# Performance work log

Measured on AMD Instinct MI355X. Metric: run time of the kernel, lower is better.

## Reference

```python
import jax, jax.numpy as jnp
import numpy as np

N = 50000
E = 800000
IN_FT = 256
OUT_FT = 64


def setup_inputs() -> dict:
    key = jax.random.key(0)
    k_seq, k_w, k_src, k_dst, k_val = jax.random.split(key, 5)
    seq = jax.random.normal(k_seq, (N, IN_FT), dtype=jnp.float32)
    # xavier_uniform_ for fc.weight [out_ft, in_ft]
    limit = float(np.sqrt(6.0 / (IN_FT + OUT_FT)))
    W = jax.random.uniform(k_w, (OUT_FT, IN_FT), minval=-limit, maxval=limit, dtype=jnp.float32)
    bias = jnp.zeros((OUT_FT,), dtype=jnp.float32)          # bias.data.fill_(0.0)
    alpha = jnp.full((1,), 0.25, dtype=jnp.float32)         # PReLU default init
    edge_src = jax.random.randint(k_src, (E,), 0, N, dtype=jnp.int32)
    edge_dst = jax.random.randint(k_dst, (E,), 0, N, dtype=jnp.int32)
    edge_val = jax.random.uniform(k_val, (E,), dtype=jnp.float32)
    return {"seq": seq, "W": W, "bias": bias, "alpha": alpha,
            "edge_src": edge_src, "edge_dst": edge_dst, "edge_val": edge_val}


def reference(seq, W, bias, alpha, edge_src, edge_dst, edge_val):
    # fc(seq): [N, in_ft] @ [in_ft, out_ft] -> [N, out_ft]
    fts = jnp.einsum('ni,oi->no', seq, W)
    # spmm(adj, fts): gather source features, scale by edge value, scatter-add to dst
    msgs = fts[edge_src] * edge_val[:, None]                # [E, out_ft]
    out = jax.ops.segment_sum(msgs, edge_dst, num_segments=seq.shape[0])
    out = out + bias
    # PReLU with scalar (single-channel) alpha
    return jnp.where(out >= 0, out, alpha * out)
```

## Files before the change

### kernel.cpp

```cpp
#include <hip/hip_runtime.h>
#include <hip/hip_fp16.h>

#define IN_FT 256
#define OUT_FT 64

constexpr int BIN_LOG   = 7;
constexpr int BIN_NODES = 1 << BIN_LOG;
constexpr int MAX_NBIN  = 512;
constexpr int BIN_CAP   = 2560;

typedef _Float16 half8 __attribute__((ext_vector_type(8)));
typedef float    f32x4 __attribute__((ext_vector_type(4)));

__global__ __launch_bounds__(256) void gemm_mfma(
    const float* __restrict__ seq, const float* __restrict__ W,
    __half* __restrict__ fts, int N, int* __restrict__ binCursor, int NBIN)
{
    const int t = (int)threadIdx.x;
    if (blockIdx.x == 0) {
        for (int i = t; i < NBIN; i += 256) binCursor[i] = 0;
    }

    __shared__ half8 Wh[4 * 8 * 64];

#pragma unroll
    for (int i = 0; i < 8; ++i) {
        int item = i * 256 + t;
        int l  = item & 63;
        int kc = (item >> 6) & 7;
        int nt = item >> 9;
        int m  = l & 15;
        int q  = l >> 4;
        const float* wp = W + (size_t)(nt * 16 + m) * IN_FT + kc * 32 + q * 8;
        float4 w0 = *(const float4*)wp;
        float4 w1 = *(const float4*)(wp + 4);
        half8 h;
        h[0] = (_Float16)w0.x; h[1] = (_Float16)w0.y;
        h[2] = (_Float16)w0.z; h[3] = (_Float16)w0.w;
        h[4] = (_Float16)w1.x; h[5] = (_Float16)w1.y;
        h[6] = (_Float16)w1.z; h[7] = (_Float16)w1.w;
        Wh[item] = h;
    }
    __syncthreads();

    const int wave = t >> 6;
    const int l    = t & 63;
    int nodeBase = (int)blockIdx.x * 64 + wave * 16;
    const bool active = (nodeBase < N);
    if (nodeBase > N - 16) nodeBase = N - 16;
    const int m = l & 15;
    const int q = l >> 4;
    const float* ap = seq + (size_t)(nodeBase + m) * IN_FT + q * 8;

    f32x4 acc0 = {0.f, 0.f, 0.f, 0.f};
    f32x4 acc1 = {0.f, 0.f, 0.f, 0.f};
    f32x4 acc2 = {0.f, 0.f, 0.f, 0.f};
    f32x4 acc3 = {0.f, 0.f, 0.f, 0.f};

    float4 a0 = *(const float4*)(ap);
    float4 a1 = *(const float4*)(ap + 4);

#pragma unroll
    for (int kc = 0; kc < 8; ++kc) {
        float4 c0 = a0, c1 = a1;
        if (kc < 7) {
            a0 = *(const float4*)(ap + (kc + 1) * 32);
            a1 = *(const float4*)(ap + (kc + 1) * 32 + 4);
        }
        half8 af;
        af[0] = (_Float16)c0.x; af[1] = (_Float16)c0.y;
        af[2] = (_Float16)c0.z; af[3] = (_Float16)c0.w;
        af[4] = (_Float16)c1.x; af[5] = (_Float16)c1.y;
        af[6] = (_Float16)c1.z; af[7] = (_Float16)c1.w;

        half8 b0 = Wh[(0 * 8 + kc) * 64 + l];
        half8 b1 = Wh[(1 * 8 + kc) * 64 + l];
        half8 b2 = Wh[(2 * 8 + kc) * 64 + l];
        half8 b3 = Wh[(3 * 8 + kc) * 64 + l];
        acc0 = __builtin_amdgcn_mfma_f32_16x16x32_f16(af, b0, acc0, 0, 0, 0);
        acc1 = __builtin_amdgcn_mfma_f32_16x16x32_f16(af, b1, acc1, 0, 0, 0);
        acc2 = __builtin_amdgcn_mfma_f32_16x16x32_f16(af, b2, acc2, 0, 0, 0);
        acc3 = __builtin_amdgcn_mfma_f32_16x16x32_f16(af, b3, acc3, 0, 0, 0);
    }

    if (active) {
#pragma unroll
        for (int r = 0; r < 4; ++r) {
            int node = nodeBase + q * 4 + r;
            __half* op = fts + (size_t)node * OUT_FT + m;
            op[0]  = __float2half(acc0[r]);
            op[16] = __float2half(acc1[r]);
            op[32] = __float2half(acc2[r]);
            op[48] = __float2half(acc3[r]);
        }
    }
}

__global__ __launch_bounds__(256) void bin_scatter(
    const int* __restrict__ src, const int* __restrict__ dst,
    const float* __restrict__ val, int* __restrict__ binCursor,
    int2* __restrict__ binned, int E, int NBIN)
{
    __shared__ int h[MAX_NBIN];
    __shared__ int base[MAX_NBIN];
    const int t = (int)threadIdx.x;
    for (int i = t; i < NBIN; i += 256) h[i] = 0;
    __syncthreads();
    const int chunk = (E + (int)gridDim.x - 1) / (int)gridDim.x;
    const int s0 = (int)blockIdx.x * chunk;
    const int e0 = min(s0 + chunk, E);
    for (int i = s0 + t; i < e0; i += 256) atomicAdd(&h[dst[i] >> BIN_LOG], 1);
    __syncthreads();
    for (int i = t; i < NBIN; i += 256) {
        int c = h[i];
        base[i] = c ? atomicAdd(&binCursor[i], c) : 0;
        h[i] = 0;
    }
    __syncthreads();
    for (int i = s0 + t; i < e0; i += 256) {
        int d = dst[i];
        int b = d >> BIN_LOG;
        int pos = base[b] + atomicAdd(&h[b], 1);
        if (pos < BIN_CAP) {
            int2 pr;
            pr.x = src[i] | ((d & (BIN_NODES - 1)) << 16);
            pr.y = __float_as_int(val[i]);
            binned[(size_t)b * BIN_CAP + pos] = pr;
        }
    }
}

__device__ __forceinline__ int block_excl_scan_256(int v, int t) {
    int lane = t & 63, wv = t >> 6;
    int incl = v;
#pragma unroll
    for (int d = 1; d < 64; d <<= 1) {
        int u = __shfl_up(incl, d, 64);
        if (lane >= d) incl += u;
    }
    __shared__ int wsum[4];
    if (lane == 63) wsum[wv] = incl;
    __syncthreads();
    int woff = 0;
    for (int i = 0; i < wv; ++i) woff += wsum[i];
    return woff + incl - v;
}

__global__ __launch_bounds__(256) void bin_scan(
    const int* __restrict__ binCursor, int* __restrict__ binStart,
    int* __restrict__ offsets, int NBIN, int N, int E)
{
    const int t = (int)threadIdx.x;
    int v0 = (2 * t     < NBIN) ? binCursor[2 * t]     : 0;
    int v1 = (2 * t + 1 < NBIN) ? binCursor[2 * t + 1] : 0;
    int s = v0 + v1;
    int excl = block_excl_scan_256(s, t);
    if (2 * t < NBIN)     binStart[2 * t]     = excl;
    if (2 * t + 1 < NBIN) binStart[2 * t + 1] = excl + v0;
    if (t == 0) offsets[N] = E;
}

__global__ __launch_bounds__(256) void bin_sort(
    const int2* __restrict__ binned, const int* __restrict__ binCursor,
    const int* __restrict__ binStart, int* __restrict__ offsets,
    unsigned int* __restrict__ pairs, int N)
{
    __shared__ int cnt[BIN_NODES];
    __shared__ int cur[BIN_NODES];
    const int b = (int)blockIdx.x;
    const int t = (int)threadIdx.x;
    const int nodeBase = b << BIN_LOG;
    const int nrec  = min(binCursor[b], BIN_CAP);
    const int start = binStart[b];
    const int2* rec = binned + (size_t)b * BIN_CAP;

    if (t < BIN_NODES) cnt[t] = 0;
    __syncthreads();
    for (int i = t; i < nrec; i += 256) atomicAdd(&cnt[rec[i].x >> 16], 1);
    __syncthreads();
    int v = (t < BIN_NODES) ? cnt[t] : 0;
    int excl = block_excl_scan_256(v, t);
    if (t < BIN_NODES) {
        cur[t] = start + excl;
        int node = nodeBase + t;
        if (node < N) offsets[node] = start + excl;
    }
    __syncthreads();
    for (int i = t; i < nrec; i += 256) {
        int2 pr = rec[i];
        int pos = atomicAdd(&cur[pr.x >> 16], 1);
        float vv = __int_as_float(pr.y);
        pairs[pos] = (unsigned int)(pr.x & 0xFFFF) |
                     ((unsigned int)__half_as_ushort(__float2half_rn(vv)) << 16);
    }
}

__global__ __launch_bounds__(256) void gather_kernel(
    const __half* __restrict__ fts, const int* __restrict__ offsets,
    const unsigned int* __restrict__ pairs,
    const float* __restrict__ bias, const float* __restrict__ alpha,
    float* __restrict__ out, int N)
{
    int gtid = (int)blockIdx.x * 256 + (int)threadIdx.x;
    int node = gtid >> 6;
    int lane = gtid & 63;
    if (node >= N) return;
    int e0 = offsets[node];
    int deg = offsets[node + 1] - e0;
    float acc = 0.f;

    for (int base = 0; base < deg; base += 64) {
        int cnt = min(64, deg - base);
        unsigned int pReg = 0;
        if (lane < cnt) pReg = pairs[e0 + base + lane];
        int j = 0;
        for (; j + 8 <= cnt; j += 8) {
            unsigned int p[8];
            float f[8];
#pragma unroll
            for (int k = 0; k < 8; ++k)
                p[k] = (unsigned int)__shfl((int)pReg, j + k, 64);
#pragma unroll
            for (int k = 0; k < 8; ++k)
                f[k] = __half2float(fts[(size_t)(p[k] & 0xFFFFu) * OUT_FT + lane]);
#pragma unroll
            for (int k = 0; k < 8; ++k) {
                float v = __half2float(__ushort_as_half((unsigned short)(p[k] >> 16)));
                acc = fmaf(f[k], v, acc);
            }
        }
        for (; j < cnt; ++j) {
            unsigned int pj = (unsigned int)__shfl((int)pReg, j, 64);
            float fj = __half2float(fts[(size_t)(pj & 0xFFFFu) * OUT_FT + lane]);
            float vj = __half2float(__ushort_as_half((unsigned short)(pj >> 16)));
            acc = fmaf(fj, vj, acc);
        }
    }
    float o = acc + bias[lane];
    float a = alpha[0];
    out[(size_t)node * OUT_FT + lane] = (o >= 0.f) ? o : a * o;
}

extern "C" void kernel_launch(void* const* d_in, const int* in_sizes, int n_in,
                              void* d_out, int out_size, void* d_ws, size_t ws_size,
                              hipStream_t stream) {
    const float* seq      = (const float*)d_in[0];
    const float* W        = (const float*)d_in[1];
    const float* bias     = (const float*)d_in[2];
    const float* alpha    = (const float*)d_in[3];
    const int*   edge_src = (const int*)d_in[4];
    const int*   edge_dst = (const int*)d_in[5];
    const float* edge_val = (const float*)d_in[6];
    float* out = (float*)d_out;

    const int N    = in_sizes[0] / IN_FT;
    const int E    = in_sizes[4];
    const int NBIN = (N + BIN_NODES - 1) >> BIN_LOG;

    size_t off = 0;
    auto take = [&](size_t bytes) -> char* {
        char* p = (char*)d_ws + off;
        off += (bytes + 255) & ~(size_t)255;
        return p;
    };
    __half*       fts       = (__half*)take((size_t)N * OUT_FT * sizeof(__half));
    int*          binCursor = (int*)take((size_t)NBIN * sizeof(int));
    int*          binStart  = (int*)take((size_t)NBIN * sizeof(int));
    int*          offsets   = (int*)take(((size_t)N + 1) * sizeof(int));
    int2*         binned    = (int2*)take((size_t)NBIN * BIN_CAP * sizeof(int2));
    unsigned int* pairs     = (unsigned int*)take((size_t)E * sizeof(unsigned int));
    (void)ws_size;

    const int gemm_blocks = (N + 63) / 64;
    gemm_mfma<<<gemm_blocks, 256, 0, stream>>>(seq, W, fts, N, binCursor, NBIN);

    bin_scatter<<<128, 256, 0, stream>>>(
        edge_src, edge_dst, edge_val, binCursor, binned, E, NBIN);
    bin_scan<<<1, 256, 0, stream>>>(binCursor, binStart, offsets, NBIN, N, E);
    bin_sort<<<NBIN, 256, 0, stream>>>(
        binned, binCursor, binStart, offsets, pairs, N);
    gather_kernel<<<((size_t)N * 64 + 255) / 256, 256, 0, stream>>>(
        fts, offsets, pairs, bias, alpha, out, N);
}
```

Baseline: 174.5 us.

## Fuse GEMM and edge binning into one launch, fold bin scan into sort

The GEMM and the edge bin-scatter now run as two independent block ranges of a single kernel, so their work can overlap and one launch is removed. The scatter gets 256 blocks instead of 128. The single-block bin_scan kernel is dropped: each bin_sort block computes its own start by reducing binCursor over all earlier bins, which is redundant work that grows with the bin index. Zeroing binCursor moves from inside the GEMM kernel to a hipMemsetAsync, which adds a memset operation to the stream.

```diff
diff --git a/kernel.cpp b/kernel.cpp
--- a/kernel.cpp
+++ b/kernel.cpp
@@ -8,17 +8,49 @@
 constexpr int BIN_NODES = 1 << BIN_LOG;
 constexpr int MAX_NBIN  = 512;
 constexpr int BIN_CAP   = 2560;
+constexpr int SC_BLOCKS = 256;
 
 typedef _Float16 half8 __attribute__((ext_vector_type(8)));
 typedef float    f32x4 __attribute__((ext_vector_type(4)));
 
-__global__ __launch_bounds__(256) void gemm_mfma(
+__global__ __launch_bounds__(256) void fused_gemm_scatter(
     const float* __restrict__ seq, const float* __restrict__ W,
-    __half* __restrict__ fts, int N, int* __restrict__ binCursor, int NBIN)
+    __half* __restrict__ fts, int N, int G,
+    const int* __restrict__ src, const int* __restrict__ dst,
+    const float* __restrict__ val, int* __restrict__ binCursor,
+    int2* __restrict__ binned, int E, int NBIN)
 {
     const int t = (int)threadIdx.x;
-    if (blockIdx.x == 0) {
-        for (int i = t; i < NBIN; i += 256) binCursor[i] = 0;
+
+    if ((int)blockIdx.x >= G) {
+        __shared__ int h[MAX_NBIN];
+        __shared__ int base[MAX_NBIN];
+        const int sb = (int)blockIdx.x - G;
+        for (int i = t; i < NBIN; i += 256) h[i] = 0;
+        __syncthreads();
+        const int chunk = (E + SC_BLOCKS - 1) / SC_BLOCKS;
+        const int s0 = sb * chunk;
+        const int e0 = min(s0 + chunk, E);
+        for (int i = s0 + t; i < e0; i += 256) atomicAdd(&h[dst[i] >> BIN_LOG], 1);
+        __syncthreads();
+        for (int i = t; i < NBIN; i += 256) {
+            int c = h[i];
+            base[i] = c ? atomicAdd(&binCursor[i], c) : 0;
+            h[i] = 0;
+        }
+        __syncthreads();
+        for (int i = s0 + t; i < e0; i += 256) {
+            int d = dst[i];
+            int b = d >> BIN_LOG;
+            int pos = base[b] + atomicAdd(&h[b], 1);
+            if (pos < BIN_CAP) {
+                int2 pr;
+                pr.x = src[i] | ((d & (BIN_NODES - 1)) << 16);
+                pr.y = __float_as_int(val[i]);
+                binned[(size_t)b * BIN_CAP + pos] = pr;
+            }
+        }
+        return;
     }
 
     __shared__ half8 Wh[4 * 8 * 64];
@@ -34,12 +66,12 @@
         const float* wp = W + (size_t)(nt * 16 + m) * IN_FT + kc * 32 + q * 8;
         float4 w0 = *(const float4*)wp;
         float4 w1 = *(const float4*)(wp + 4);
-        half8 h;
-        h[0] = (_Float16)w0.x; h[1] = (_Float16)w0.y;
-        h[2] = (_Float16)w0.z; h[3] = (_Float16)w0.w;
-        h[4] = (_Float16)w1.x; h[5] = (_Float16)w1.y;
-        h[6] = (_Float16)w1.z; h[7] = (_Float16)w1.w;
-        Wh[item] = h;
+        half8 hh;
+        hh[0] = (_Float16)w0.x; hh[1] = (_Float16)w0.y;
+        hh[2] = (_Float16)w0.z; hh[3] = (_Float16)w0.w;
+        hh[4] = (_Float16)w1.x; hh[5] = (_Float16)w1.y;
+        hh[6] = (_Float16)w1.z; hh[7] = (_Float16)w1.w;
+        Wh[item] = hh;
     }
     __syncthreads();
 
@@ -96,40 +128,6 @@
     }
 }
 
-__global__ __launch_bounds__(256) void bin_scatter(
-    const int* __restrict__ src, const int* __restrict__ dst,
-    const float* __restrict__ val, int* __restrict__ binCursor,
-    int2* __restrict__ binned, int E, int NBIN)
-{
-    __shared__ int h[MAX_NBIN];
-    __shared__ int base[MAX_NBIN];
-    const int t = (int)threadIdx.x;
-    for (int i = t; i < NBIN; i += 256) h[i] = 0;
-    __syncthreads();
-    const int chunk = (E + (int)gridDim.x - 1) / (int)gridDim.x;
-    const int s0 = (int)blockIdx.x * chunk;
-    const int e0 = min(s0 + chunk, E);
-    for (int i = s0 + t; i < e0; i += 256) atomicAdd(&h[dst[i] >> BIN_LOG], 1);
-    __syncthreads();
-    for (int i = t; i < NBIN; i += 256) {
-        int c = h[i];
-        base[i] = c ? atomicAdd(&binCursor[i], c) : 0;
-        h[i] = 0;
-    }
-    __syncthreads();
-    for (int i = s0 + t; i < e0; i += 256) {
-        int d = dst[i];
-        int b = d >> BIN_LOG;
-        int pos = base[b] + atomicAdd(&h[b], 1);
-        if (pos < BIN_CAP) {
-            int2 pr;
-            pr.x = src[i] | ((d & (BIN_NODES - 1)) << 16);
-            pr.y = __float_as_int(val[i]);
-            binned[(size_t)b * BIN_CAP + pos] = pr;
-        }
-    }
-}
-
 __device__ __forceinline__ int block_excl_scan_256(int v, int t) {
     int lane = t & 63, wv = t >> 6;
     int incl = v;
@@ -146,36 +144,30 @@
     return woff + incl - v;
 }
 
-__global__ __launch_bounds__(256) void bin_scan(
-    const int* __restrict__ binCursor, int* __restrict__ binStart,
-    int* __restrict__ offsets, int NBIN, int N, int E)
-{
-    const int t = (int)threadIdx.x;
-    int v0 = (2 * t     < NBIN) ? binCursor[2 * t]     : 0;
-    int v1 = (2 * t + 1 < NBIN) ? binCursor[2 * t + 1] : 0;
-    int s = v0 + v1;
-    int excl = block_excl_scan_256(s, t);
-    if (2 * t < NBIN)     binStart[2 * t]     = excl;
-    if (2 * t + 1 < NBIN) binStart[2 * t + 1] = excl + v0;
-    if (t == 0) offsets[N] = E;
-}
-
 __global__ __launch_bounds__(256) void bin_sort(
     const int2* __restrict__ binned, const int* __restrict__ binCursor,
-    const int* __restrict__ binStart, int* __restrict__ offsets,
-    unsigned int* __restrict__ pairs, int N)
+    int* __restrict__ offsets, unsigned int* __restrict__ pairs,
+    int N, int E, int NBIN)
 {
     __shared__ int cnt[BIN_NODES];
     __shared__ int cur[BIN_NODES];
+    __shared__ int red[4];
     const int b = (int)blockIdx.x;
     const int t = (int)threadIdx.x;
+    const int lane = t & 63, wv = t >> 6;
     const int nodeBase = b << BIN_LOG;
+
+    int s = 0;
+    for (int i = t; i < b; i += 256) s += binCursor[i];
+#pragma unroll
+    for (int d = 32; d >= 1; d >>= 1) s += __shfl_down(s, d, 64);
+    if (lane == 0) red[wv] = s;
+    if (t < BIN_NODES) cnt[t] = 0;
+    __syncthreads();
+    const int start = red[0] + red[1] + red[2] + red[3];
     const int nrec  = min(binCursor[b], BIN_CAP);
-    const int start = binStart[b];
     const int2* rec = binned + (size_t)b * BIN_CAP;
 
-    if (t < BIN_NODES) cnt[t] = 0;
-    __syncthreads();
     for (int i = t; i < nrec; i += 256) atomicAdd(&cnt[rec[i].x >> 16], 1);
     __syncthreads();
     int v = (t < BIN_NODES) ? cnt[t] : 0;
@@ -185,6 +177,7 @@
         int node = nodeBase + t;
         if (node < N) offsets[node] = start + excl;
     }
+    if (b == NBIN - 1 && t == 0) offsets[N] = E;
     __syncthreads();
     for (int i = t; i < nrec; i += 256) {
         int2 pr = rec[i];
@@ -265,20 +258,20 @@
     };
     __half*       fts       = (__half*)take((size_t)N * OUT_FT * sizeof(__half));
     int*          binCursor = (int*)take((size_t)NBIN * sizeof(int));
-    int*          binStart  = (int*)take((size_t)NBIN * sizeof(int));
     int*          offsets   = (int*)take(((size_t)N + 1) * sizeof(int));
     int2*         binned    = (int2*)take((size_t)NBIN * BIN_CAP * sizeof(int2));
     unsigned int* pairs     = (unsigned int*)take((size_t)E * sizeof(unsigned int));
     (void)ws_size;
 
-    const int gemm_blocks = (N + 63) / 64;
-    gemm_mfma<<<gemm_blocks, 256, 0, stream>>>(seq, W, fts, N, binCursor, NBIN);
-
-    bin_scatter<<<128, 256, 0, stream>>>(
-        edge_src, edge_dst, edge_val, binCursor, binned, E, NBIN);
-    bin_scan<<<1, 256, 0, stream>>>(binCursor, binStart, offsets, NBIN, N, E);
+    hipMemsetAsync(binCursor, 0, (size_t)NBIN * sizeof(int), stream);
+
+    const int G = (N + 63) / 64;
+    fused_gemm_scatter<<<G + SC_BLOCKS, 256, 0, stream>>>(
+        seq, W, fts, N, G, edge_src, edge_dst, edge_val,
+        binCursor, binned, E, NBIN);
+
     bin_sort<<<NBIN, 256, 0, stream>>>(
-        binned, binCursor, binStart, offsets, pairs, N);
+        binned, binCursor, offsets, pairs, N, E, NBIN);
     gather_kernel<<<((size_t)N * 64 + 255) / 256, 256, 0, stream>>>(
         fts, offsets, pairs, bias, alpha, out, N);
 }
```

New measurement: 158.0 us. -9.5%, faster.
